# Performance work log

Hardware: AMD Instinct MI355X
Metric: run time of the kernel (lower is better)

Reference implementation:

```python
import jax, jax.numpy as jnp
import numpy as np

B, C, T = 64, 80, 16384
EPS = 1e-6
QS = (0.25, 0.5, 0.75)


def setup_inputs() -> dict:
    key = jax.random.key(0)
    k1, k2 = jax.random.split(key)
    x = jax.random.normal(k1, (B, C, T), dtype=jnp.float32)
    lengths = jax.random.randint(k2, (B,), T // 2, T + 1, dtype=jnp.int32)
    return {"x": x, "lengths": lengths}


def _stat_pool(x, lengths):
    # x: (B, C, T), lengths: (B,)
    t = jnp.arange(x.shape[-1])
    valid = t[None, :] < lengths[:, None]          # (B, T) bool
    mask = valid[:, None, :].astype(x.dtype)       # (B, 1, T)
    denom = jnp.clip(mask.sum(axis=2), EPS)        # (B, 1)
    mean = (x * mask).sum(axis=2) / denom          # (B, C)
    var = (((x - mean[..., None]) ** 2) * mask).sum(axis=2) / denom
    std = jnp.sqrt(jnp.clip(var, EPS))             # (B, C)

    # Quantiles over valid prefix: push pads to +inf, sort once, gather+lerp.
    x_pad = jnp.where(valid[:, None, :], x, jnp.inf)
    xs = jnp.sort(x_pad, axis=2)                   # (B, C, T), valid values first
    n1 = (lengths - 1).astype(x.dtype)             # (B,) = n-1

    def quantile(q):
        pos = q * n1                               # (B,) fractional index
        lo = jnp.floor(pos).astype(jnp.int32)
        hi = jnp.ceil(pos).astype(jnp.int32)
        w = (pos - lo.astype(x.dtype))[:, None]    # (B, 1)
        xlo = jnp.take_along_axis(xs, lo[:, None, None], axis=2)[..., 0]  # (B, C)
        xhi = jnp.take_along_axis(xs, hi[:, None, None], axis=2)[..., 0]
        return xlo + w * (xhi - xlo)               # torch.quantile 'linear'

    q25, q50, q75 = (quantile(q) for q in QS)
    return jnp.concatenate([mean, std, q25, q50, q75], axis=1)  # (B, 5*C)


def reference(x, lengths):
    return _stat_pool(x, lengths)
```

## Files before the change

kernel.cpp:

```cpp
#include <hip/hip_runtime.h>
#include <stdint.h>

#define BB 64
#define CC 80
#define TT 16384
#define NB 2048
#define CAP 1024
#define NT 256

__device__ __forceinline__ int bucket_of(float v) {
    float bf = fmaf(v, 256.0f, 1024.0f);
    bf = fminf(fmaxf(bf, 0.0f), 2047.0f);
    return (int)bf;
}

extern "C" __global__ __launch_bounds__(NT)
void statpool(const float* __restrict__ x, const int* __restrict__ lengths,
              float* __restrict__ out) {
    const int row = blockIdx.x;
    const int b   = row / CC;
    const int c   = row % CC;
    const float* __restrict__ xr = x + (size_t)row * TT;
    const int L   = lengths[b];
    const int tid = threadIdx.x;
    const int lane = tid & 63;
    const int wid  = tid >> 6;

    __shared__ uint32_t hist[NB];
    __shared__ float    cand[CAP];
    __shared__ uint32_t tsum[NT];
    __shared__ float    wsum[4], wsq[4];
    __shared__ int      rbkt[6], rwr[6];
    __shared__ float    wts[3];
    __shared__ uint32_t ccount;

    for (int i = tid; i < NB; i += NT) hist[i] = 0u;
    __syncthreads();

    float sum = 0.f, sq = 0.f;
    const int nfull = L >> 2;
    const float4* x4 = (const float4*)xr;
    for (int i = tid; i < nfull; i += NT) {
        float4 v = x4[i];
        sum += v.x + v.y + v.z + v.w;
        sq  = fmaf(v.x, v.x, fmaf(v.y, v.y, fmaf(v.z, v.z, fmaf(v.w, v.w, sq))));
        atomicAdd(&hist[bucket_of(v.x)], 1u);
        atomicAdd(&hist[bucket_of(v.y)], 1u);
        atomicAdd(&hist[bucket_of(v.z)], 1u);
        atomicAdd(&hist[bucket_of(v.w)], 1u);
    }
    if (tid < (L & 3)) {
        float v = xr[(L & ~3) + tid];
        sum += v; sq = fmaf(v, v, sq);
        atomicAdd(&hist[bucket_of(v)], 1u);
    }
    for (int off = 32; off > 0; off >>= 1) {
        sum += __shfl_down(sum, off);
        sq  += __shfl_down(sq,  off);
    }
    if (lane == 0) { wsum[wid] = sum; wsq[wid] = sq; }
    __syncthreads();

    uint32_t v8[NB / NT];
    {
        uint32_t s = 0;
        const int base = tid * (NB / NT);
        #pragma unroll
        for (int i = 0; i < NB / NT; i++) { v8[i] = hist[base + i]; s += v8[i]; }
        tsum[tid] = s;
    }
    __syncthreads();

    if (tid == 0) {
        uint32_t r = 0;
        for (int i = 0; i < NT; i++) { uint32_t t = tsum[i]; tsum[i] = r; r += t; }
        float fs = wsum[0] + wsum[1] + wsum[2] + wsum[3];
        float fq = wsq[0]  + wsq[1]  + wsq[2]  + wsq[3];
        float denom = (float)L;
        float mean = fs / denom;
        float var  = fq / denom - mean * mean;
        float stdv = sqrtf(fmaxf(var, 1e-6f));
        out[(size_t)b * (5*CC) + 0*CC + c] = mean;
        out[(size_t)b * (5*CC) + 1*CC + c] = stdv;
        ccount = 0u;
    }
    __syncthreads();

    {
        const int base = tid * (NB / NT);
        uint32_t run = tsum[tid];
        #pragma unroll
        for (int i = 0; i < NB / NT; i++) { run += v8[i]; hist[base + i] = run; }
    }
    __syncthreads();

    if (tid < 6) {
        const float qs3[3] = {0.25f, 0.5f, 0.75f};
        const int qi = tid >> 1;
        float pos = qs3[qi] * (float)(L - 1);
        int r = (tid & 1) ? (int)ceilf(pos) : (int)floorf(pos);
        if ((tid & 1) == 0) wts[qi] = pos - floorf(pos);
        int lo = 0, hi = NB - 1;
        while (lo < hi) {
            int mid = (lo + hi) >> 1;
            if (hist[mid] > (uint32_t)r) hi = mid; else lo = mid + 1;
        }
        rbkt[tid] = lo;
        rwr[tid]  = r - (int)(lo ? hist[lo - 1] : 0u);
    }
    __syncthreads();

    const int b0 = rbkt[0], b1 = rbkt[1], b2 = rbkt[2],
              b3 = rbkt[3], b4 = rbkt[4], b5 = rbkt[5];

    auto gthr = [&](float f) {
        int bk = bucket_of(f);
        if (bk == b0 || bk == b1 || bk == b2 || bk == b3 || bk == b4 || bk == b5) {
            uint32_t p = atomicAdd(&ccount, 1u);
            if (p < CAP) cand[p] = f;
        }
    };
    for (int i = tid; i < nfull; i += NT) {
        float4 v = x4[i];
        gthr(v.x); gthr(v.y); gthr(v.z); gthr(v.w);
    }
    if (tid < (L & 3)) gthr(xr[(L & ~3) + tid]);
    __syncthreads();

    int m = (int)(ccount < (uint32_t)CAP ? ccount : (uint32_t)CAP);
    int n = 1; while (n < m) n <<= 1;
    for (int i = m + tid; i < n; i += NT) cand[i] = __builtin_inff();
    __syncthreads();

    for (int k = 2; k <= n; k <<= 1) {
        for (int j = k >> 1; j > 0; j >>= 1) {
            for (int i = tid; i < n; i += NT) {
                int ixj = i ^ j;
                if (ixj > i) {
                    float a = cand[i], bv = cand[ixj];
                    bool asc = ((i & k) == 0);
                    if (asc ? (a > bv) : (a < bv)) { cand[i] = bv; cand[ixj] = a; }
                }
            }
            __syncthreads();
        }
    }

    if (tid < 3) {
        const int jl = 2 * tid, jh = 2 * tid + 1;
        int bkl = rbkt[jl];
        int lo = 0, hi = n;
        while (lo < hi) { int mid = (lo + hi) >> 1; if (bucket_of(cand[mid]) < bkl) lo = mid + 1; else hi = mid; }
        float xlo = cand[lo + rwr[jl]];
        int bkh = rbkt[jh];
        lo = 0; hi = n;
        while (lo < hi) { int mid = (lo + hi) >> 1; if (bucket_of(cand[mid]) < bkh) lo = mid + 1; else hi = mid; }
        float xhi = cand[lo + rwr[jh]];
        float val = xlo + wts[tid] * (xhi - xlo);
        out[(size_t)b * (5*CC) + (2 + tid) * CC + c] = val;
    }
}

extern "C" void kernel_launch(void* const* d_in, const int* in_sizes, int n_in,
                              void* d_out, int out_size, void* d_ws, size_t ws_size,
                              hipStream_t stream) {
    (void)in_sizes; (void)n_in; (void)out_size; (void)d_ws; (void)ws_size;
    const float* x       = (const float*)d_in[0];
    const int*   lengths = (const int*)d_in[1];
    float*       out     = (float*)d_out;
    hipLaunchKernelGGL(statpool, dim3(BB * CC), dim3(NT), 0, stream, x, lengths, out);
}
```

Baseline: 465.3 us.

## Keep each row in registers across both passes and parallelize the bucket prefix scan

Each thread now loads its whole slice of the row (16 float4s) into registers once and reuses it for the stats/histogram pass and the candidate-gather pass. This removes the second global read of x. The serial single-thread prefix over 256 partial sums becomes a wave-level shuffle scan, and the gather test changes from six equality checks to three range checks. It also sets launch bounds to request 4 blocks per CU. The cost is high register pressure (64 floats per thread plus the rest), which may force spills or lower occupancy.

```diff
diff --git a/kernel.cpp b/kernel.cpp
--- a/kernel.cpp
+++ b/kernel.cpp
@@ -7,6 +7,7 @@
 #define NB 2048
 #define CAP 1024
 #define NT 256
+#define VPT 16
 
 __device__ __forceinline__ int bucket_of(float v) {
     float bf = fmaf(v, 256.0f, 1024.0f);
@@ -14,7 +15,7 @@
     return (int)bf;
 }
 
-extern "C" __global__ __launch_bounds__(NT)
+extern "C" __global__ __launch_bounds__(NT, 4)
 void statpool(const float* __restrict__ x, const int* __restrict__ lengths,
               float* __restrict__ out) {
     const int row = blockIdx.x;
@@ -37,22 +38,36 @@
     for (int i = tid; i < NB; i += NT) hist[i] = 0u;
     __syncthreads();
 
-    float sum = 0.f, sq = 0.f;
     const int nfull = L >> 2;
     const float4* x4 = (const float4*)xr;
-    for (int i = tid; i < nfull; i += NT) {
-        float4 v = x4[i];
-        sum += v.x + v.y + v.z + v.w;
-        sq  = fmaf(v.x, v.x, fmaf(v.y, v.y, fmaf(v.z, v.z, fmaf(v.w, v.w, sq))));
-        atomicAdd(&hist[bucket_of(v.x)], 1u);
-        atomicAdd(&hist[bucket_of(v.y)], 1u);
-        atomicAdd(&hist[bucket_of(v.z)], 1u);
-        atomicAdd(&hist[bucket_of(v.w)], 1u);
-    }
-    if (tid < (L & 3)) {
-        float v = xr[(L & ~3) + tid];
-        sum += v; sq = fmaf(v, v, sq);
-        atomicAdd(&hist[bucket_of(v)], 1u);
+    float4 v4[VPT];
+    #pragma unroll
+    for (int i = 0; i < VPT; i++) {
+        int idx = tid + i * NT;
+        v4[i] = make_float4(0.f, 0.f, 0.f, 0.f);
+        if (idx < nfull) v4[i] = x4[idx];
+    }
+    float tailv = 0.f;
+    const bool hasTail = tid < (L & 3);
+    if (hasTail) tailv = xr[(L & ~3) + tid];
+
+    float sum = 0.f, sq = 0.f;
+    #pragma unroll
+    for (int i = 0; i < VPT; i++) {
+        int idx = tid + i * NT;
+        if (idx < nfull) {
+            float4 v = v4[i];
+            sum += v.x + v.y + v.z + v.w;
+            sq  = fmaf(v.x, v.x, fmaf(v.y, v.y, fmaf(v.z, v.z, fmaf(v.w, v.w, sq))));
+            atomicAdd(&hist[bucket_of(v.x)], 1u);
+            atomicAdd(&hist[bucket_of(v.y)], 1u);
+            atomicAdd(&hist[bucket_of(v.z)], 1u);
+            atomicAdd(&hist[bucket_of(v.w)], 1u);
+        }
+    }
+    if (hasTail) {
+        sum += tailv; sq = fmaf(tailv, tailv, sq);
+        atomicAdd(&hist[bucket_of(tailv)], 1u);
     }
     for (int off = 32; off > 0; off >>= 1) {
         sum += __shfl_down(sum, off);
@@ -61,19 +76,31 @@
     if (lane == 0) { wsum[wid] = sum; wsq[wid] = sq; }
     __syncthreads();
 
-    uint32_t v8[NB / NT];
+    const int base = tid * (NB / NT);
     {
         uint32_t s = 0;
-        const int base = tid * (NB / NT);
         #pragma unroll
-        for (int i = 0; i < NB / NT; i++) { v8[i] = hist[base + i]; s += v8[i]; }
+        for (int i = 0; i < NB / NT; i++) s += hist[base + i];
         tsum[tid] = s;
     }
     __syncthreads();
 
-    if (tid == 0) {
-        uint32_t r = 0;
-        for (int i = 0; i < NT; i++) { uint32_t t = tsum[i]; tsum[i] = r; r += t; }
+    if (tid < 64) {
+        uint32_t a0 = tsum[4*tid+0], a1 = tsum[4*tid+1],
+                 a2 = tsum[4*tid+2], a3 = tsum[4*tid+3];
+        uint32_t tot = a0 + a1 + a2 + a3;
+        uint32_t inc = tot;
+        #pragma unroll
+        for (int off = 1; off < 64; off <<= 1) {
+            uint32_t t = __shfl_up(inc, off);
+            if (tid >= off) inc += t;
+        }
+        uint32_t ex = inc - tot;
+        tsum[4*tid+0] = ex;
+        tsum[4*tid+1] = ex + a0;
+        tsum[4*tid+2] = ex + a0 + a1;
+        tsum[4*tid+3] = ex + a0 + a1 + a2;
+    } else if (tid == 64) {
         float fs = wsum[0] + wsum[1] + wsum[2] + wsum[3];
         float fq = wsq[0]  + wsq[1]  + wsq[2]  + wsq[3];
         float denom = (float)L;
@@ -87,10 +114,9 @@
     __syncthreads();
 
     {
-        const int base = tid * (NB / NT);
         uint32_t run = tsum[tid];
         #pragma unroll
-        for (int i = 0; i < NB / NT; i++) { run += v8[i]; hist[base + i] = run; }
+        for (int i = 0; i < NB / NT; i++) { run += hist[base + i]; hist[base + i] = run; }
     }
     __syncthreads();
 
@@ -115,16 +141,22 @@
 
     auto gthr = [&](float f) {
         int bk = bucket_of(f);
-        if (bk == b0 || bk == b1 || bk == b2 || bk == b3 || bk == b4 || bk == b5) {
+        bool hit = (bk >= b0 && bk <= b1) || (bk >= b2 && bk <= b3) ||
+                   (bk >= b4 && bk <= b5);
+        if (hit) {
             uint32_t p = atomicAdd(&ccount, 1u);
             if (p < CAP) cand[p] = f;
         }
     };
-    for (int i = tid; i < nfull; i += NT) {
-        float4 v = x4[i];
-        gthr(v.x); gthr(v.y); gthr(v.z); gthr(v.w);
-    }
-    if (tid < (L & 3)) gthr(xr[(L & ~3) + tid]);
+    #pragma unroll
+    for (int i = 0; i < VPT; i++) {
+        int idx = tid + i * NT;
+        if (idx < nfull) {
+            float4 v = v4[i];
+            gthr(v.x); gthr(v.y); gthr(v.z); gthr(v.w);
+        }
+    }
+    if (hasTail) gthr(tailv);
     __syncthreads();
 
     int m = (int)(ccount < (uint32_t)CAP ? ccount : (uint32_t)CAP);
```

Measured after the change: 448.8 us. 3.6% less time.
